# Performance work log

Hardware: AMD Instinct MI355X
Metric: run time of the kernel (lower is better)

## Reference

```python
import jax, jax.numpy as jnp
import numpy as np

N_HIDDEN = 100  # module-level global n_hidden in source
LN_EPS = 1e-5


def _layernorm(x, g, b):
    mu = jnp.mean(x, axis=-1, keepdims=True)
    var = jnp.mean(jnp.square(x - mu), axis=-1, keepdims=True)
    return (x - mu) * jax.lax.rsqrt(var + LN_EPS) * g + b


def setup_inputs() -> dict:
    key = jax.random.key(0)
    B, T, C, H = 8, 1024, 768, 12
    D = C // H  # head_size = 64
    ks = jax.random.split(key, 12)
    s_qkv = 1.0 / np.sqrt(C)
    s_ff1 = 1.0 / np.sqrt(C)
    s_ff2 = 1.0 / np.sqrt(N_HIDDEN)
    return {
        "x": jax.random.normal(ks[0], (B, T, C), dtype=jnp.float32),
        # per-head K/Q/V projections stacked: [H, C, D]
        "Wq": jax.random.uniform(ks[1], (H, C, D), jnp.float32, -s_qkv, s_qkv),
        "Wk": jax.random.uniform(ks[2], (H, C, D), jnp.float32, -s_qkv, s_qkv),
        "Wv": jax.random.uniform(ks[3], (H, C, D), jnp.float32, -s_qkv, s_qkv),
        "Wproj": jax.random.uniform(ks[4], (C, C), jnp.float32, -s_qkv, s_qkv),
        "bproj": jnp.zeros((C,), jnp.float32),
        "ln1_g": jnp.ones((C,), jnp.float32),
        "ln1_b": jnp.zeros((C,), jnp.float32),
        "W1": jax.random.uniform(ks[5], (C, N_HIDDEN), jnp.float32, -s_ff1, s_ff1),
        "b1": jnp.zeros((N_HIDDEN,), jnp.float32),
        "W2": jax.random.uniform(ks[6], (N_HIDDEN, C), jnp.float32, -s_ff2, s_ff2),
        "b2": jnp.zeros((C,), jnp.float32),
        "ln2_g": jnp.ones((C,), jnp.float32),
        "ln2_b": jnp.zeros((C,), jnp.float32),
    }


def reference(x, Wq, Wk, Wv, Wproj, bproj, ln1_g, ln1_b, W1, b1, W2, b2, ln2_g, ln2_b):
    B, T, C = x.shape
    # batched-over-heads QKV (source does a Python loop per head; same math)
    q = jnp.einsum('btc,hcd->bhtd', x, Wq)
    k = jnp.einsum('btc,hcd->bhtd', x, Wk)
    v = jnp.einsum('btc,hcd->bhtd', x, Wv)
    # NOTE: source scales by C**-0.5 where C = n_embd (not head_size)
    wei = jnp.einsum('bhtd,bhsd->bhts', q, k) * (C ** -0.5)
    wei = jax.nn.softmax(wei, axis=-1)  # attn_maps, returned
    out = jnp.einsum('bhts,bhsd->bhtd', wei, v)
    out = out.transpose(0, 2, 1, 3).reshape(B, T, C)  # concat heads
    attn_out = out @ Wproj + bproj
    h = _layernorm(x + attn_out, ln1_g, ln1_b)
    ff = jax.nn.relu(h @ W1 + b1) @ W2 + b2
    y = _layernorm(h + ff, ln2_g, ln2_b)
    return (wei, y)
```

## Files before the change

### kernel.cpp

```cpp
#include <hip/hip_runtime.h>
#include <hip/hip_bf16.h>
#include <cstdint>

typedef __bf16 bf16_t;
typedef __bf16 bf16x8 __attribute__((ext_vector_type(8)));
typedef __bf16 bf16x4 __attribute__((ext_vector_type(4)));
typedef float f32x4 __attribute__((ext_vector_type(4)));

#define B_ 8
#define T_ 1024
#define C_ 768
#define H_ 12
#define D_ 64
#define NTOK 8192
#define NHID_PAD 128
#define SCALE 0.03608439182435161f
#define WEI_ELEMS 100663296ull

__device__ __forceinline__ f32x4 mfma16(bf16x8 a, bf16x8 b, f32x4 c) {
    return __builtin_amdgcn_mfma_f32_16x16x32_bf16(a, b, c, 0, 0, 0);
}

__global__ __launch_bounds__(256) void k_cast_x(const float* __restrict__ x,
                                                bf16_t* __restrict__ xb) {
    int i = blockIdx.x * 256 + threadIdx.x;
    const float4 v = reinterpret_cast<const float4*>(x)[i];
    bf16x4 o;
    o.x = (bf16_t)v.x; o.y = (bf16_t)v.y; o.z = (bf16_t)v.z; o.w = (bf16_t)v.w;
    *reinterpret_cast<bf16x4*>(xb + 4 * i) = o;
}

__global__ __launch_bounds__(256) void k_pack_qkv(const float* __restrict__ Wq,
                                                  const float* __restrict__ Wk,
                                                  const float* __restrict__ Wv,
                                                  bf16_t* __restrict__ out) {
    int idx = blockIdx.x * 256 + threadIdx.x;
    int row = idx / C_, c = idx - row * C_;
    int p = row / C_;
    int hd = row - p * C_;
    int h = hd >> 6, d = hd & 63;
    const float* W = (p == 0) ? Wq : (p == 1 ? Wk : Wv);
    out[idx] = (bf16_t)W[((size_t)h * C_ + c) * D_ + d];
}

__global__ __launch_bounds__(256) void k_pack_proj(const float* __restrict__ W,
                                                   bf16_t* __restrict__ out) {
    int idx = blockIdx.x * 256 + threadIdx.x;
    int n = idx / C_, k = idx - n * C_;
    out[idx] = (bf16_t)W[(size_t)k * C_ + n];
}

__global__ __launch_bounds__(256) void k_pack_w1(const float* __restrict__ W,
                                                 bf16_t* __restrict__ out) {
    int idx = blockIdx.x * 256 + threadIdx.x;
    int n = idx / C_, k = idx - n * C_;
    out[idx] = (bf16_t)((n < 100) ? W[(size_t)k * 100 + n] : 0.0f);
}

__global__ __launch_bounds__(256) void k_pack_w2(const float* __restrict__ W,
                                                 bf16_t* __restrict__ out) {
    int idx = blockIdx.x * 256 + threadIdx.x;
    int n = idx / NHID_PAD, k = idx & (NHID_PAD - 1);
    out[idx] = (bf16_t)((k < 100) ? W[(size_t)k * C_ + n] : 0.0f);
}

__device__ __forceinline__ void gemm_core(const bf16_t* __restrict__ A, int lda,
                                          const bf16_t* __restrict__ B, int ldb,
                                          int K, f32x4 acc[4][4]) {
    __shared__ __align__(16) bf16_t As[128 * 40];
    __shared__ __align__(16) bf16_t Bs[128 * 40];
    const int tid = threadIdx.x;
    const int wave = tid >> 6, lane = tid & 63;
    const int q = lane >> 4, ln = lane & 15;
    const int wm = (wave >> 1) * 64, wn = (wave & 1) * 64;
    const size_t bm = (size_t)blockIdx.y * 128, bn = (size_t)blockIdx.x * 128;

    const int lrow = tid >> 2;
    const int lkg = (tid & 3) * 8;

    const bf16_t* Ap0 = A + (bm + lrow) * lda + lkg;
    const bf16_t* Ap1 = A + (bm + lrow + 64) * lda + lkg;
    const bf16_t* Bp0 = B + (bn + lrow) * ldb + lkg;
    const bf16_t* Bp1 = B + (bn + lrow + 64) * ldb + lkg;
    bf16_t* As0 = &As[lrow * 40 + lkg];
    bf16_t* As1 = &As[(lrow + 64) * 40 + lkg];
    bf16_t* Bs0 = &Bs[lrow * 40 + lkg];
    bf16_t* Bs1 = &Bs[(lrow + 64) * 40 + lkg];

    for (int k0 = 0; k0 < K; k0 += 32) {
        bf16x8 a0 = *reinterpret_cast<const bf16x8*>(Ap0 + k0);
        bf16x8 a1 = *reinterpret_cast<const bf16x8*>(Ap1 + k0);
        bf16x8 b0 = *reinterpret_cast<const bf16x8*>(Bp0 + k0);
        bf16x8 b1 = *reinterpret_cast<const bf16x8*>(Bp1 + k0);
        __syncthreads();
        *reinterpret_cast<bf16x8*>(As0) = a0;
        *reinterpret_cast<bf16x8*>(As1) = a1;
        *reinterpret_cast<bf16x8*>(Bs0) = b0;
        *reinterpret_cast<bf16x8*>(Bs1) = b1;
        __syncthreads();
        bf16x8 af[4], bfr[4];
#pragma unroll
        for (int i = 0; i < 4; ++i)
            af[i] = *reinterpret_cast<const bf16x8*>(&As[(wm + i * 16 + ln) * 40 + q * 8]);
#pragma unroll
        for (int j = 0; j < 4; ++j)
            bfr[j] = *reinterpret_cast<const bf16x8*>(&Bs[(wn + j * 16 + ln) * 40 + q * 8]);
#pragma unroll
        for (int i = 0; i < 4; ++i)
#pragma unroll
            for (int j = 0; j < 4; ++j)
                acc[i][j] = mfma16(af[i], bfr[j], acc[i][j]);
    }
}

#define EPI_PROLOG                                              \
    const int lane = threadIdx.x & 63;                          \
    const int wave = threadIdx.x >> 6;                          \
    const int q = lane >> 4, ln = lane & 15;                    \
    const int row0 = blockIdx.y * 128 + (wave >> 1) * 64;       \
    const int col0 = blockIdx.x * 128 + (wave & 1) * 64;

__global__ __launch_bounds__(256) void k_gemm_qk(const bf16_t* __restrict__ A,
                                                 const bf16_t* __restrict__ Bm,
                                                 bf16_t* __restrict__ qb,
                                                 bf16_t* __restrict__ kb) {
    f32x4 acc[4][4] = {};
    gemm_core(A, C_, Bm, C_, C_, acc);
    EPI_PROLOG
#pragma unroll
    for (int i = 0; i < 4; ++i)
#pragma unroll
        for (int j = 0; j < 4; ++j)
#pragma unroll
            for (int r = 0; r < 4; ++r) {
                int grow = row0 + i * 16 + q * 4 + r;
                int gcol = col0 + j * 16 + ln;
                int p = (gcol >= C_) ? 1 : 0;
                int c = gcol - p * C_;
                int h = c >> 6, d = c & 63;
                int b = grow >> 10, t = grow & 1023;
                bf16_t* dst = p ? kb : qb;
                dst[(((size_t)b * H_ + h) * T_ + t) * D_ + d] = (bf16_t)acc[i][j][r];
            }
}

__global__ __launch_bounds__(256) void k_gemm_vt(const bf16_t* __restrict__ A,
                                                 const bf16_t* __restrict__ Bm,
                                                 bf16_t* __restrict__ vt) {
    f32x4 acc[4][4] = {};
    gemm_core(A, C_, Bm, C_, C_, acc);
    EPI_PROLOG
#pragma unroll
    for (int i = 0; i < 4; ++i)
#pragma unroll
        for (int j = 0; j < 4; ++j)
#pragma unroll
            for (int r = 0; r < 4; ++r) {
                int grow = row0 + i * 16 + q * 4 + r;
                int gcol = col0 + j * 16 + ln;
                int h = grow >> 6, d = grow & 63;
                int b = gcol >> 10, t = gcol & 1023;
                vt[(((size_t)b * H_ + h) * D_ + d) * T_ + t] = (bf16_t)acc[i][j][r];
            }
}

__global__ __launch_bounds__(256) void k_gemm_proj(const bf16_t* __restrict__ A,
                                                   const bf16_t* __restrict__ Bm,
                                                   const float* __restrict__ bias,
                                                   float* __restrict__ out) {
    f32x4 acc[4][4] = {};
    gemm_core(A, C_, Bm, C_, C_, acc);
    EPI_PROLOG
#pragma unroll
    for (int i = 0; i < 4; ++i)
#pragma unroll
        for (int j = 0; j < 4; ++j)
#pragma unroll
            for (int r = 0; r < 4; ++r) {
                int grow = row0 + i * 16 + q * 4 + r;
                int gcol = col0 + j * 16 + ln;
                out[(size_t)grow * C_ + gcol] = acc[i][j][r] + bias[gcol];
            }
}

__global__ __launch_bounds__(256) void k_gemm_ff1(const bf16_t* __restrict__ A,
                                                  const bf16_t* __restrict__ Bm,
                                                  const float* __restrict__ bias,
                                                  bf16_t* __restrict__ out) {
    f32x4 acc[4][4] = {};
    gemm_core(A, C_, Bm, C_, C_, acc);
    EPI_PROLOG
#pragma unroll
    for (int i = 0; i < 4; ++i)
#pragma unroll
        for (int j = 0; j < 4; ++j)
#pragma unroll
            for (int r = 0; r < 4; ++r) {
                int grow = row0 + i * 16 + q * 4 + r;
                int gcol = col0 + j * 16 + ln;
                float v = acc[i][j][r] + ((gcol < 100) ? bias[gcol] : 0.0f);
                v = fmaxf(v, 0.0f);
                out[(size_t)grow * NHID_PAD + gcol] = (bf16_t)v;
            }
}

__global__ __launch_bounds__(256) void k_gemm_ff2(const bf16_t* __restrict__ A,
                                                  const bf16_t* __restrict__ Bm,
                                                  const float* __restrict__ bias,
                                                  float* __restrict__ out) {
    f32x4 acc[4][4] = {};
    gemm_core(A, NHID_PAD, Bm, NHID_PAD, NHID_PAD, acc);
    EPI_PROLOG
#pragma unroll
    for (int i = 0; i < 4; ++i)
#pragma unroll
        for (int j = 0; j < 4; ++j)
#pragma unroll
            for (int r = 0; r < 4; ++r) {
                int grow = row0 + i * 16 + q * 4 + r;
                int gcol = col0 + j * 16 + ln;
                out[(size_t)grow * C_ + gcol] = acc[i][j][r] + bias[gcol];
            }
}

__global__ __launch_bounds__(256) void k_attn(const bf16_t* __restrict__ qb,
                                              const bf16_t* __restrict__ kb,
                                              const bf16_t* __restrict__ vt,
                                              float* __restrict__ wei,
                                              bf16_t* __restrict__ attn) {
    __shared__ __align__(16) bf16_t Qs[32 * 72];
    __shared__ __align__(16) bf16_t Ks[128 * 72];
    __shared__ __align__(16) bf16_t Vts[64 * 136];
    __shared__ __align__(16) bf16_t Sb[32 * 1032];

    const int tid = threadIdx.x;
    const int wave = tid >> 6, lane = tid & 63, q = lane >> 4, ln = lane & 15;
    const int bh = blockIdx.y;
    const int b = bh / H_, h = bh - b * H_;
    const int t0 = blockIdx.x * 32;
    const size_t bhbase = (size_t)bh * T_ * D_;

    {
        int r = tid >> 3, dg = (tid & 7) * 8;
        *reinterpret_cast<bf16x8*>(&Qs[r * 72 + dg]) =
            *reinterpret_cast<const bf16x8*>(qb + bhbase + (size_t)(t0 + r) * D_ + dg);
    }

    for (int st = 0; st < 8; ++st) {
        int s0 = st * 128;
#pragma unroll
        for (int u = 0; u < 4; ++u) {
            int l = u * 256 + tid;
            int r = l >> 3, dg = (l & 7) * 8;
            *reinterpret_cast<bf16x8*>(&Ks[r * 72 + dg]) =
                *reinterpret_cast<const bf16x8*>(kb + bhbase + (size_t)(s0 + r) * D_ + dg);
        }
        __syncthreads();
        f32x4 sacc[2][2] = {};
#pragma unroll
        for (int ks = 0; ks < 2; ++ks) {
            int ko = ks * 32 + q * 8;
            bf16x8 a0 = *reinterpret_cast<const bf16x8*>(&Qs[ln * 72 + ko]);
            bf16x8 a1 = *reinterpret_cast<const bf16x8*>(&Qs[(16 + ln) * 72 + ko]);
            bf16x8 b0 = *reinterpret_cast<const bf16x8*>(&Ks[(wave * 32 + ln) * 72 + ko]);
            bf16x8 b1 = *reinterpret_cast<const bf16x8*>(&Ks[(wave * 32 + 16 + ln) * 72 + ko]);
            sacc[0][0] = mfma16(a0, b0, sacc[0][0]);
            sacc[0][1] = mfma16(a0, b1, sacc[0][1]);
            sacc[1][0] = mfma16(a1, b0, sacc[1][0]);
            sacc[1][1] = mfma16(a1, b1, sacc[1][1]);
        }
#pragma unroll
        for (int i = 0; i < 2; ++i)
#pragma unroll
            for (int jj = 0; jj < 2; ++jj)
#pragma unroll
                for (int r = 0; r < 4; ++r) {
                    int row = i * 16 + q * 4 + r;
                    int col = s0 + wave * 32 + jj * 16 + ln;
                    Sb[row * 1032 + col] = (bf16_t)(sacc[i][jj][r] * SCALE);
                }
        __syncthreads();
    }

    for (int rr = 0; rr < 8; ++rr) {
        int row = wave * 8 + rr;
        bf16_t* srow = &Sb[row * 1032];
        float vv[16];
        float mx = -1e30f;
#pragma unroll
        for (int jj = 0; jj < 16; ++jj) {
            vv[jj] = (float)srow[jj * 64 + lane];
            mx = fmaxf(mx, vv[jj]);
        }
#pragma unroll
        for (int off = 32; off; off >>= 1) mx = fmaxf(mx, __shfl_xor(mx, off));
        float sum = 0.0f;
#pragma unroll
        for (int jj = 0; jj < 16; ++jj) {
            vv[jj] = __expf(vv[jj] - mx);
            sum += vv[jj];
        }
#pragma unroll
        for (int off = 32; off; off >>= 1) sum += __shfl_xor(sum, off);
        float inv = 1.0f / sum;
        float* wrow = wei + ((size_t)bh << 20) + (size_t)(t0 + row) * T_;
#pragma unroll
        for (int jj = 0; jj < 16; ++jj) {
            float p = vv[jj] * inv;
            wrow[jj * 64 + lane] = p;
            srow[jj * 64 + lane] = (bf16_t)p;
        }
    }
    __syncthreads();

    f32x4 oacc[2] = {};
    const size_t vbase = (size_t)bh * D_ * T_;
    for (int st = 0; st < 8; ++st) {
        int s0 = st * 128;
#pragma unroll
        for (int u = 0; u < 4; ++u) {
            int l = u * 256 + tid;
            int d = l >> 4, sg = (l & 15) * 8;
            *reinterpret_cast<bf16x8*>(&Vts[d * 136 + sg]) =
                *reinterpret_cast<const bf16x8*>(vt + vbase + (size_t)d * T_ + s0 + sg);
        }
        __syncthreads();
#pragma unroll
        for (int ks = 0; ks < 4; ++ks) {
            int ko = ks * 32 + q * 8;
            bf16x8 b0 = *reinterpret_cast<const bf16x8*>(&Vts[(wave * 16 + ln) * 136 + ko]);
            bf16x8 a0 = *reinterpret_cast<const bf16x8*>(&Sb[ln * 1032 + s0 + ko]);
            bf16x8 a1 = *reinterpret_cast<const bf16x8*>(&Sb[(16 + ln) * 1032 + s0 + ko]);
            oacc[0] = mfma16(a0, b0, oacc[0]);
            oacc[1] = mfma16(a1, b0, oacc[1]);
        }
        __syncthreads();
    }
#pragma unroll
    for (int i = 0; i < 2; ++i)
#pragma unroll
        for (int r = 0; r < 4; ++r) {
            int trow = t0 + i * 16 + q * 4 + r;
            int col = h * D_ + wave * 16 + ln;
            attn[((size_t)b * T_ + trow) * C_ + col] = (bf16_t)oacc[i][r];
        }
}

__global__ __launch_bounds__(256) void k_ln(const float* __restrict__ a,
                                            const float* __restrict__ bsrc,
                                            const float* __restrict__ g,
                                            const float* __restrict__ beta,
                                            float* __restrict__ of,
                                            bf16_t* __restrict__ ob) {
    int row = blockIdx.x;
    int tid = threadIdx.x;
    const float* pa = a + (size_t)row * C_;
    const float* pb = bsrc + (size_t)row * C_;
    float v[3];
    float s = 0.0f, s2 = 0.0f;
#pragma unroll
    for (int u = 0; u < 3; ++u) {
        int c = tid + u * 256;
        v[u] = pa[c] + pb[c];
        s += v[u];
        s2 += v[u] * v[u];
    }
#pragma unroll
    for (int off = 32; off; off >>= 1) {
        s += __shfl_down(s, off);
        s2 += __shfl_down(s2, off);
    }
    __shared__ float ws[4], ws2[4];
    if ((tid & 63) == 0) { ws[tid >> 6] = s; ws2[tid >> 6] = s2; }
    __syncthreads();
    s = ws[0] + ws[1] + ws[2] + ws[3];
    s2 = ws2[0] + ws2[1] + ws2[2] + ws2[3];
    float mu = s * (1.0f / C_);
    float var = s2 * (1.0f / C_) - mu * mu;
    float ri = rsqrtf(var + 1e-5f);
#pragma unroll
    for (int u = 0; u < 3; ++u) {
        int c = tid + u * 256;
        float y = (v[u] - mu) * ri * g[c] + beta[c];
        of[(size_t)row * C_ + c] = y;
        if (ob) ob[(size_t)row * C_ + c] = (bf16_t)y;
    }
}

extern "C" void kernel_launch(void* const* d_in, const int* in_sizes, int n_in,
                              void* d_out, int out_size, void* d_ws, size_t ws_size,
                              hipStream_t stream) {
    const float* x     = (const float*)d_in[0];
    const float* Wq    = (const float*)d_in[1];
    const float* Wk    = (const float*)d_in[2];
    const float* Wv    = (const float*)d_in[3];
    const float* Wproj = (const float*)d_in[4];
    const float* bproj = (const float*)d_in[5];
    const float* ln1g  = (const float*)d_in[6];
    const float* ln1b  = (const float*)d_in[7];
    const float* W1    = (const float*)d_in[8];
    const float* b1    = (const float*)d_in[9];
    const float* W2    = (const float*)d_in[10];
    const float* b2    = (const float*)d_in[11];
    const float* ln2g  = (const float*)d_in[12];
    const float* ln2b  = (const float*)d_in[13];

    char* ws = (char*)d_ws;
    bf16_t* xb     = (bf16_t*)(ws + 0);
    bf16_t* wqkvt  = (bf16_t*)(ws + 12582912);
    bf16_t* qbuf   = (bf16_t*)(ws + 16121856);
    bf16_t* kbuf   = (bf16_t*)(ws + 28704768);
    bf16_t* vtb    = (bf16_t*)(ws + 41287680);
    bf16_t* attnb  = (bf16_t*)(ws + 53870592);
    bf16_t* wprojt = (bf16_t*)(ws + 66453504);
    float*  projb  = (float*)(ws + 67633152);
    float*  hbuf   = (float*)(ws + 92798976);
    bf16_t* hidb   = (bf16_t*)(ws + 117964800);
    bf16_t* w1t    = (bf16_t*)(ws + 120061952);
    bf16_t* w2t    = (bf16_t*)(ws + 120258560);
    bf16_t* hbb    = xb;
    float*  ffb    = projb;

    float* wei = (float*)d_out;
    float* y   = (float*)d_out + WEI_ELEMS;

    k_cast_x<<<6144, 256, 0, stream>>>(x, xb);
    k_pack_qkv<<<6912, 256, 0, stream>>>(Wq, Wk, Wv, wqkvt);
    k_pack_proj<<<2304, 256, 0, stream>>>(Wproj, wprojt);
    k_pack_w1<<<384, 256, 0, stream>>>(W1, w1t);
    k_pack_w2<<<384, 256, 0, stream>>>(W2, w2t);

    k_gemm_qk<<<dim3(12, 64), 256, 0, stream>>>(xb, wqkvt, qbuf, kbuf);
    k_gemm_vt<<<dim3(64, 6), 256, 0, stream>>>(wqkvt + (size_t)1536 * C_, xb, vtb);

    k_attn<<<dim3(32, 96), 256, 0, stream>>>(qbuf, kbuf, vtb, wei, attnb);

    k_gemm_proj<<<dim3(6, 64), 256, 0, stream>>>(attnb, wprojt, bproj, projb);
    k_ln<<<8192, 256, 0, stream>>>(x, projb, ln1g, ln1b, hbuf, hbb);
    k_gemm_ff1<<<dim3(1, 64), 256, 0, stream>>>(hbb, w1t, b1, hidb);
    k_gemm_ff2<<<dim3(6, 64), 256, 0, stream>>>(hidb, w2t, b2, ffb);
    k_ln<<<8192, 256, 0, stream>>>(hbuf, ffb, ln2g, ln2b, y, (bf16_t*)nullptr);

    (void)in_sizes; (void)n_in; (void)out_size; (void)ws_size;
}
```

Measured before the change: 853.2 us.

## Restructure attention to keep scores in registers and use direct global-to-LDS GEMM loads

The attention kernel is rewritten to process 16 query rows per block. Each wave computes QK^T for 256 keys straight from global memory into registers, and softmax runs in fp32 registers with cross-wave reductions through shared memory, removing the bf16 round-trip of scores through LDS. The PV product reads V directly from global memory, and the grid doubles to 64x96 with a launch bound targeting 3 blocks per CU. The GEMM core now uses global_load_lds to copy tiles directly into unpadded shared memory, avoiding register staging but risking LDS bank conflicts. K/V are reloaded per block from global memory (more L2 traffic), and softmax now runs on fp32 scores instead of bf16, which changes numerics slightly.

Result: faster. 764.9 us (-10.3%).

```diff
diff --git a/kernel.cpp b/kernel.cpp
--- a/kernel.cpp
+++ b/kernel.cpp
@@ -19,6 +19,12 @@
 
 __device__ __forceinline__ f32x4 mfma16(bf16x8 a, bf16x8 b, f32x4 c) {
     return __builtin_amdgcn_mfma_f32_16x16x32_bf16(a, b, c, 0, 0, 0);
+}
+
+typedef const unsigned int __attribute__((address_space(1)))* gaddr_t;
+typedef unsigned int __attribute__((address_space(3)))* laddr_t;
+__device__ __forceinline__ void gload16(const bf16_t* g, bf16_t* l) {
+    __builtin_amdgcn_global_load_lds((gaddr_t)g, (laddr_t)l, 16, 0, 0);
 }
 
 __global__ __launch_bounds__(256) void k_cast_x(const float* __restrict__ x,
@@ -67,44 +73,40 @@
 __device__ __forceinline__ void gemm_core(const bf16_t* __restrict__ A, int lda,
                                           const bf16_t* __restrict__ B, int ldb,
                                           int K, f32x4 acc[4][4]) {
-    __shared__ __align__(16) bf16_t As[128 * 40];
-    __shared__ __align__(16) bf16_t Bs[128 * 40];
+    __shared__ __align__(16) bf16_t As[128 * 32];
+    __shared__ __align__(16) bf16_t Bs[128 * 32];
     const int tid = threadIdx.x;
     const int wave = tid >> 6, lane = tid & 63;
     const int q = lane >> 4, ln = lane & 15;
     const int wm = (wave >> 1) * 64, wn = (wave & 1) * 64;
     const size_t bm = (size_t)blockIdx.y * 128, bn = (size_t)blockIdx.x * 128;
 
-    const int lrow = tid >> 2;
-    const int lkg = (tid & 3) * 8;
-
-    const bf16_t* Ap0 = A + (bm + lrow) * lda + lkg;
-    const bf16_t* Ap1 = A + (bm + lrow + 64) * lda + lkg;
-    const bf16_t* Bp0 = B + (bn + lrow) * ldb + lkg;
-    const bf16_t* Bp1 = B + (bn + lrow + 64) * ldb + lkg;
-    bf16_t* As0 = &As[lrow * 40 + lkg];
-    bf16_t* As1 = &As[(lrow + 64) * 40 + lkg];
-    bf16_t* Bs0 = &Bs[lrow * 40 + lkg];
-    bf16_t* Bs1 = &Bs[(lrow + 64) * 40 + lkg];
+    const int c0 = wave * 2;
+    const int srow = c0 * 16 + (lane >> 2);
+    const int kg = (lane & 3) * 8;
+    const bf16_t* Ap0 = A + (bm + srow) * lda + kg;
+    const bf16_t* Ap1 = A + (bm + srow + 16) * lda + kg;
+    const bf16_t* Bp0 = B + (bn + srow) * ldb + kg;
+    const bf16_t* Bp1 = B + (bn + srow + 16) * ldb + kg;
+    bf16_t* AsD0 = As + c0 * 512;
+    bf16_t* AsD1 = As + (c0 + 1) * 512;
+    bf16_t* BsD0 = Bs + c0 * 512;
+    bf16_t* BsD1 = Bs + (c0 + 1) * 512;
 
     for (int k0 = 0; k0 < K; k0 += 32) {
-        bf16x8 a0 = *reinterpret_cast<const bf16x8*>(Ap0 + k0);
-        bf16x8 a1 = *reinterpret_cast<const bf16x8*>(Ap1 + k0);
-        bf16x8 b0 = *reinterpret_cast<const bf16x8*>(Bp0 + k0);
-        bf16x8 b1 = *reinterpret_cast<const bf16x8*>(Bp1 + k0);
         __syncthreads();
-        *reinterpret_cast<bf16x8*>(As0) = a0;
-        *reinterpret_cast<bf16x8*>(As1) = a1;
-        *reinterpret_cast<bf16x8*>(Bs0) = b0;
-        *reinterpret_cast<bf16x8*>(Bs1) = b1;
+        gload16(Ap0 + k0, AsD0);
+        gload16(Ap1 + k0, AsD1);
+        gload16(Bp0 + k0, BsD0);
+        gload16(Bp1 + k0, BsD1);
         __syncthreads();
         bf16x8 af[4], bfr[4];
 #pragma unroll
         for (int i = 0; i < 4; ++i)
-            af[i] = *reinterpret_cast<const bf16x8*>(&As[(wm + i * 16 + ln) * 40 + q * 8]);
-#pragma unroll
-        for (int j = 0; j < 4; ++j)
-            bfr[j] = *reinterpret_cast<const bf16x8*>(&Bs[(wn + j * 16 + ln) * 40 + q * 8]);
+            af[i] = *reinterpret_cast<const bf16x8*>(&As[(wm + i * 16 + ln) * 32 + q * 8]);
+#pragma unroll
+        for (int j = 0; j < 4; ++j)
+            bfr[j] = *reinterpret_cast<const bf16x8*>(&Bs[(wn + j * 16 + ln) * 32 + q * 8]);
 #pragma unroll
         for (int i = 0; i < 4; ++i)
 #pragma unroll
@@ -223,127 +225,112 @@
             }
 }
 
-__global__ __launch_bounds__(256) void k_attn(const bf16_t* __restrict__ qb,
-                                              const bf16_t* __restrict__ kb,
-                                              const bf16_t* __restrict__ vt,
-                                              float* __restrict__ wei,
-                                              bf16_t* __restrict__ attn) {
-    __shared__ __align__(16) bf16_t Qs[32 * 72];
-    __shared__ __align__(16) bf16_t Ks[128 * 72];
-    __shared__ __align__(16) bf16_t Vts[64 * 136];
-    __shared__ __align__(16) bf16_t Sb[32 * 1032];
+__global__ __launch_bounds__(256, 3) void k_attn(const bf16_t* __restrict__ qb,
+                                                 const bf16_t* __restrict__ kb,
+                                                 const bf16_t* __restrict__ vt,
+                                                 float* __restrict__ wei,
+                                                 bf16_t* __restrict__ attn) {
+    __shared__ __align__(16) bf16_t Ps[16 * 1032];
+    __shared__ float redm[4][16];
+    __shared__ float reds[4][16];
 
     const int tid = threadIdx.x;
-    const int wave = tid >> 6, lane = tid & 63, q = lane >> 4, ln = lane & 15;
+    const int w = tid >> 6, lane = tid & 63;
+    const int qq = lane >> 4, ln = lane & 15;
     const int bh = blockIdx.y;
     const int b = bh / H_, h = bh - b * H_;
-    const int t0 = blockIdx.x * 32;
-    const size_t bhbase = (size_t)bh * T_ * D_;
-
-    {
-        int r = tid >> 3, dg = (tid & 7) * 8;
-        *reinterpret_cast<bf16x8*>(&Qs[r * 72 + dg]) =
-            *reinterpret_cast<const bf16x8*>(qb + bhbase + (size_t)(t0 + r) * D_ + dg);
-    }
-
-    for (int st = 0; st < 8; ++st) {
-        int s0 = st * 128;
-#pragma unroll
-        for (int u = 0; u < 4; ++u) {
-            int l = u * 256 + tid;
-            int r = l >> 3, dg = (l & 7) * 8;
-            *reinterpret_cast<bf16x8*>(&Ks[r * 72 + dg]) =
-                *reinterpret_cast<const bf16x8*>(kb + bhbase + (size_t)(s0 + r) * D_ + dg);
+    const int t0 = blockIdx.x * 16;
+    const size_t bhbase = (size_t)bh * (T_ * D_);
+
+    const bf16_t* qp = qb + bhbase + (size_t)(t0 + ln) * D_ + qq * 8;
+    const bf16x8 aq0 = *reinterpret_cast<const bf16x8*>(qp);
+    const bf16x8 aq1 = *reinterpret_cast<const bf16x8*>(qp + 32);
+
+    f32x4 sacc[16] = {};
+    const bf16_t* kp = kb + bhbase + (size_t)(w * 256 + ln) * D_ + qq * 8;
+#pragma unroll
+    for (int j = 0; j < 16; ++j) {
+        bf16x8 b0 = *reinterpret_cast<const bf16x8*>(kp + j * 16 * D_);
+        bf16x8 b1 = *reinterpret_cast<const bf16x8*>(kp + j * 16 * D_ + 32);
+        sacc[j] = mfma16(aq0, b0, sacc[j]);
+        sacc[j] = mfma16(aq1, b1, sacc[j]);
+    }
+
+    float mx[4];
+#pragma unroll
+    for (int r = 0; r < 4; ++r) {
+        float m = sacc[0][r];
+#pragma unroll
+        for (int j = 1; j < 16; ++j) m = fmaxf(m, sacc[j][r]);
+#pragma unroll
+        for (int off = 1; off < 16; off <<= 1) m = fmaxf(m, __shfl_xor(m, off));
+        mx[r] = m;
+    }
+    if (ln == 0) {
+#pragma unroll
+        for (int r = 0; r < 4; ++r) redm[w][qq * 4 + r] = mx[r];
+    }
+    __syncthreads();
+#pragma unroll
+    for (int r = 0; r < 4; ++r) {
+        int row = qq * 4 + r;
+        mx[r] = fmaxf(fmaxf(redm[0][row], redm[1][row]),
+                      fmaxf(redm[2][row], redm[3][row]));
+    }
+
+    float rs[4] = {0.0f, 0.0f, 0.0f, 0.0f};
+#pragma unroll
+    for (int j = 0; j < 16; ++j)
+#pragma unroll
+        for (int r = 0; r < 4; ++r) {
+            float p = __expf((sacc[j][r] - mx[r]) * SCALE);
+            sacc[j][r] = p;
+            rs[r] += p;
         }
-        __syncthreads();
-        f32x4 sacc[2][2] = {};
-#pragma unroll
-        for (int ks = 0; ks < 2; ++ks) {
-            int ko = ks * 32 + q * 8;
-            bf16x8 a0 = *reinterpret_cast<const bf16x8*>(&Qs[ln * 72 + ko]);
-            bf16x8 a1 = *reinterpret_cast<const bf16x8*>(&Qs[(16 + ln) * 72 + ko]);
-            bf16x8 b0 = *reinterpret_cast<const bf16x8*>(&Ks[(wave * 32 + ln) * 72 + ko]);
-            bf16x8 b1 = *reinterpret_cast<const bf16x8*>(&Ks[(wave * 32 + 16 + ln) * 72 + ko]);
-            sacc[0][0] = mfma16(a0, b0, sacc[0][0]);
-            sacc[0][1] = mfma16(a0, b1, sacc[0][1]);
-            sacc[1][0] = mfma16(a1, b0, sacc[1][0]);
-            sacc[1][1] = mfma16(a1, b1, sacc[1][1]);
+#pragma unroll
+    for (int r = 0; r < 4; ++r)
+#pragma unroll
+        for (int off = 1; off < 16; off <<= 1) rs[r] += __shfl_xor(rs[r], off);
+    if (ln == 0) {
+#pragma unroll
+        for (int r = 0; r < 4; ++r) reds[w][qq * 4 + r] = rs[r];
+    }
+    __syncthreads();
+    float inv[4];
+#pragma unroll
+    for (int r = 0; r < 4; ++r) {
+        int row = qq * 4 + r;
+        inv[r] = 1.0f / (reds[0][row] + reds[1][row] + reds[2][row] + reds[3][row]);
+    }
+
+    float* wbase = wei + ((size_t)bh << 20) + (size_t)t0 * T_ + w * 256 + ln;
+#pragma unroll
+    for (int r = 0; r < 4; ++r) {
+        int row = qq * 4 + r;
+        float* wr = wbase + (size_t)row * T_;
+        bf16_t* pr = &Ps[row * 1032 + w * 256 + ln];
+#pragma unroll
+        for (int j = 0; j < 16; ++j) {
+            float p = sacc[j][r] * inv[r];
+            wr[j * 16] = p;
+            pr[j * 16] = (bf16_t)p;
         }
-#pragma unroll
-        for (int i = 0; i < 2; ++i)
-#pragma unroll
-            for (int jj = 0; jj < 2; ++jj)
-#pragma unroll
-                for (int r = 0; r < 4; ++r) {
-                    int row = i * 16 + q * 4 + r;
-                    int col = s0 + wave * 32 + jj * 16 + ln;
-                    Sb[row * 1032 + col] = (bf16_t)(sacc[i][jj][r] * SCALE);
-                }
-        __syncthreads();
-    }
-
-    for (int rr = 0; rr < 8; ++rr) {
-        int row = wave * 8 + rr;
-        bf16_t* srow = &Sb[row * 1032];
-        float vv[16];
-        float mx = -1e30f;
-#pragma unroll
-        for (int jj = 0; jj < 16; ++jj) {
-            vv[jj] = (float)srow[jj * 64 + lane];
-            mx = fmaxf(mx, vv[jj]);
-        }
-#pragma unroll
-        for (int off = 32; off; off >>= 1) mx = fmaxf(mx, __shfl_xor(mx, off));
-        float sum = 0.0f;
-#pragma unroll
-        for (int jj = 0; jj < 16; ++jj) {
-            vv[jj] = __expf(vv[jj] - mx);
-            sum += vv[jj];
-        }
-#pragma unroll
-        for (int off = 32; off; off >>= 1) sum += __shfl_xor(sum, off);
-        float inv = 1.0f / sum;
-        float* wrow = wei + ((size_t)bh << 20) + (size_t)(t0 + row) * T_;
-#pragma unroll
-        for (int jj = 0; jj < 16; ++jj) {
-            float p = vv[jj] * inv;
-            wrow[jj * 64 + lane] = p;
-            srow[jj * 64 + lane] = (bf16_t)p;
-        }
     }
     __syncthreads();
 
-    f32x4 oacc[2] = {};
-    const size_t vbase = (size_t)bh * D_ * T_;
-    for (int st = 0; st < 8; ++st) {
-        int s0 = st * 128;
-#pragma unroll
-        for (int u = 0; u < 4; ++u) {
-            int l = u * 256 + tid;
-            int d = l >> 4, sg = (l & 15) * 8;
-            *reinterpret_cast<bf16x8*>(&Vts[d * 136 + sg]) =
-                *reinterpret_cast<const bf16x8*>(vt + vbase + (size_t)d * T_ + s0 + sg);
-        }
-        __syncthreads();
-#pragma unroll
-        for (int ks = 0; ks < 4; ++ks) {
-            int ko = ks * 32 + q * 8;
-            bf16x8 b0 = *reinterpret_cast<const bf16x8*>(&Vts[(wave * 16 + ln) * 136 + ko]);
-            bf16x8 a0 = *reinterpret_cast<const bf16x8*>(&Sb[ln * 1032 + s0 + ko]);
-            bf16x8 a1 = *reinterpret_cast<const bf16x8*>(&Sb[(16 + ln) * 1032 + s0 + ko]);
-            oacc[0] = mfma16(a0, b0, oacc[0]);
-            oacc[1] = mfma16(a1, b0, oacc[1]);
-        }
-        __syncthreads();
-    }
-#pragma unroll
-    for (int i = 0; i < 2; ++i)
-#pragma unroll
-        for (int r = 0; r < 4; ++r) {
-            int trow = t0 + i * 16 + q * 4 + r;
-            int col = h * D_ + wave * 16 + ln;
-            attn[((size_t)b * T_ + trow) * C_ + col] = (bf16_t)oacc[i][r];
-        }
+    f32x4 oacc = {};
+    const bf16_t* vp = vt + (size_t)bh * (D_ * T_) + (size_t)(w * 16 + ln) * T_ + qq * 8;
+#pragma unroll
+    for (int ks = 0; ks < 32; ++ks) {
+        bf16x8 a = *reinterpret_cast<const bf16x8*>(&Ps[ln * 1032 + ks * 32 + qq * 8]);
+        bf16x8 bv = *reinterpret_cast<const bf16x8*>(vp + ks * 32);
+        oacc = mfma16(a, bv, oacc);
+    }
+#pragma unroll
+    for (int r = 0; r < 4; ++r) {
+        int trow = t0 + qq * 4 + r;
+        attn[((size_t)b * T_ + trow) * C_ + h * D_ + w * 16 + ln] = (bf16_t)oacc[r];
+    }
 }
 
 __global__ __launch_bounds__(256) void k_ln(const float* __restrict__ a,
@@ -433,7 +420,7 @@
     k_gemm_qk<<<dim3(12, 64), 256, 0, stream>>>(xb, wqkvt, qbuf, kbuf);
     k_gemm_vt<<<dim3(64, 6), 256, 0, stream>>>(wqkvt + (size_t)1536 * C_, xb, vtb);
 
-    k_attn<<<dim3(32, 96), 256, 0, stream>>>(qbuf, kbuf, vtb, wei, attnb);
+    k_attn<<<dim3(64, 96), 256, 0, stream>>>(qbuf, kbuf, vtb, wei, attnb);
 
     k_gemm_proj<<<dim3(6, 64), 256, 0, stream>>>(attnb, wprojt, bproj, projb);
     k_ln<<<8192, 256, 0, stream>>>(x, projb, ln1g, ln1b, hbuf, hbb);
```
